# Performance work log

Measured on AMD Instinct MI355X. Metric: run time of the kernel, lower is better.

Reference implementation:

```python
import jax, jax.numpy as jnp
import numpy as np

B, T, N, K, d = 8, 12, 325, 8, 64
D = K * d


def setup_inputs() -> dict:
    key = jax.random.key(0)
    ks = jax.random.split(key, 12)
    s = 0.02
    f32 = jnp.float32
    inp = {
        "X": jax.random.normal(ks[0], (B, T, N, D), f32),
        "STE": jax.random.normal(ks[1], (B, T, N, D), f32),
        "Wq": (jax.random.normal(ks[2], (2 * D, D), f32) * s),
        "bq": jnp.zeros((D,), f32),
        "Wk": (jax.random.normal(ks[3], (2 * D, D), f32) * s),
        "bk": jnp.zeros((D,), f32),
        "Wv": (jax.random.normal(ks[4], (2 * D, D), f32) * s),
        "bv": jnp.zeros((D,), f32),
        "W1": (jax.random.normal(ks[5], (D, D), f32) * s),
        "b1": jnp.zeros((D,), f32),
        "W2": (jax.random.normal(ks[6], (D, D), f32) * s),
        "b2": jnp.zeros((D,), f32),
        "attn_mask": 0,
    }
    return inp


def reference(X, STE, Wq, bq, Wk, bk, Wv, bv, W1, b1, W2, b2, attn_mask):
    # X, STE: [B, T, N, D]
    Xc = jnp.concatenate([X, STE], axis=-1)          # [B,T,N,2D]
    q = jax.nn.relu(Xc @ Wq + bq).reshape(B, T, N, K, d)
    k = jax.nn.relu(Xc @ Wk + bk).reshape(B, T, N, K, d)
    v = jax.nn.relu(Xc @ Wv + bv).reshape(B, T, N, K, d)

    # scores: [B, K, T, N, N] (attention over spatial/node axis N)
    scores = jnp.einsum('btnhe,btmhe->bhtnm', q, k)
    # mask_flag=False -> TriangularCausalMask applied (upper-tri masked with -inf)
    causal = jnp.triu(jnp.ones((N, N), dtype=bool), 1)
    scores = jnp.where(causal, -jnp.inf, scores)
    # original scales AFTER masking; -inf / sqrt(d) stays -inf
    scores = scores / jnp.sqrt(jnp.asarray(d, scores.dtype))
    attn = jax.nn.softmax(scores, axis=-1)
    # dropout: eval mode (identity)

    ctx = jnp.einsum('bhtnm,btmhe->btnhe', attn, v).reshape(B, T, N, D)
    out = jax.nn.relu(ctx @ W1 + b1) @ W2 + b2        # [B,T,N,D]

    # match torch's head-major cat(dim=0): [K*B, T, N, N]
    attn_full = jnp.transpose(attn, (1, 0, 2, 3, 4)).reshape(K * B, T, N, N)
    return out, attn_full
```

## Files before the change

kernel.cpp:

```cpp
#include <hip/hip_runtime.h>
#include <hip/hip_bf16.h>

typedef __hip_bfloat16 bf16;
using f32x4  = __attribute__((ext_vector_type(4))) float;
using short8 = __attribute__((ext_vector_type(8))) short;

#define M_ROWS   31200
#define M_PAD    31232
#define N_TOK    325
#define D_MODEL  512
#define QKV_LD   1536
#define VTG_LD   336

#define GLOBAL_AS(p) ((const __attribute__((address_space(1))) unsigned int*)(p))
#define LDS_AS(p)    ((__attribute__((address_space(3))) unsigned int*)(p))

__global__ void init_flag(int* flag) { if (threadIdx.x == 0) *flag = 0; }

__global__ void detect_dtype(const unsigned short* __restrict__ x, int* flag)
{
    int i = blockIdx.x * 256 + threadIdx.x;
    unsigned short h = x[i];
    int e = (h >> 7) & 0xFF;
    if (e >= 135) atomicOr(flag, 1);
}

__device__ __forceinline__ float load_in(const void* p, size_t i, bool f32)
{
    return f32 ? ((const float*)p)[i] : __bfloat162float(((const bf16*)p)[i]);
}

__global__ void concat_cast(const void* __restrict__ X, const void* __restrict__ STE,
                            bf16* __restrict__ Xc, const int* __restrict__ flag)
{
    const bool f32 = (*flag != 0);
    int idx = blockIdx.x * 256 + threadIdx.x;
    int r = idx >> 7, c8 = (idx & 127) << 3;
    short8 v = {0, 0, 0, 0, 0, 0, 0, 0};
    if (r < M_ROWS) {
        const void* src = (c8 < 512) ? X : STE;
        int cc = c8 & 511;
        if (f32) {
            const float* s = (const float*)src + (size_t)r * 512 + cc;
            float4 a = *(const float4*)s;
            float4 b = *(const float4*)(s + 4);
            ((bf16*)&v)[0] = __float2bfloat16(a.x); ((bf16*)&v)[1] = __float2bfloat16(a.y);
            ((bf16*)&v)[2] = __float2bfloat16(a.z); ((bf16*)&v)[3] = __float2bfloat16(a.w);
            ((bf16*)&v)[4] = __float2bfloat16(b.x); ((bf16*)&v)[5] = __float2bfloat16(b.y);
            ((bf16*)&v)[6] = __float2bfloat16(b.z); ((bf16*)&v)[7] = __float2bfloat16(b.w);
        } else {
            v = *(const short8*)((const bf16*)src + (size_t)r * 512 + cc);
        }
    }
    *(short8*)&Xc[(size_t)r * 1024 + c8] = v;
}

__global__ void transpose_w_tiled(const void* __restrict__ src, bf16* __restrict__ dst,
                                  int krows, int ncols, const int* __restrict__ flag)
{
    __shared__ float tile[32][33];
    const bool f32 = (*flag != 0);
    const int kt = blockIdx.y * 32, nt = blockIdx.x * 32;
    const int tx = threadIdx.x & 31, ty = threadIdx.x >> 5;
#pragma unroll
    for (int r = 0; r < 32; r += 8)
        tile[ty + r][tx] = load_in(src, (size_t)(kt + ty + r) * ncols + (nt + tx), f32);
    __syncthreads();
#pragma unroll
    for (int r = 0; r < 32; r += 8)
        dst[(size_t)(nt + ty + r) * krows + (kt + tx)] = __float2bfloat16(tile[tx][ty + r]);
}

__global__ void prep_bias(const void* __restrict__ bq, const void* __restrict__ bk,
                          const void* __restrict__ bv, const void* __restrict__ b1,
                          const void* __restrict__ b2,
                          float* __restrict__ biasQKV, float* __restrict__ b1f,
                          float* __restrict__ b2f, const int* __restrict__ flag)
{
    const bool f32 = (*flag != 0);
    int i = blockIdx.x * 256 + threadIdx.x;
    if (i < 512) {
        biasQKV[i]        = load_in(bq, i, f32);
        biasQKV[512 + i]  = load_in(bk, i, f32);
        biasQKV[1024 + i] = load_in(bv, i, f32);
        b1f[i] = load_in(b1, i, f32);
        b2f[i] = load_in(b2, i, f32);
    }
}

__global__ void vt_transpose(const bf16* __restrict__ qkv, bf16* __restrict__ vtg)
{
    __shared__ bf16 vs[N_TOK * 72];
    const int t = threadIdx.x;
    const int h = blockIdx.x & 7, bt = blockIdx.x >> 3;
    const size_t rowbase = (size_t)bt * N_TOK;
    for (int task = t; task < N_TOK * 8; task += 256) {
        int m = task >> 3, e0 = (task & 7) << 3;
        *(short8*)&vs[m * 72 + e0] =
            *(const short8*)(qkv + (rowbase + m) * QKV_LD + 1024 + h * 64 + e0);
    }
    __syncthreads();
    bf16* dst = vtg + (size_t)blockIdx.x * 64 * VTG_LD;
    for (int task = t; task < 64 * VTG_LD; task += 256) {
        int e = task / VTG_LD, m = task % VTG_LD;
        dst[task] = (m < N_TOK) ? vs[m * 72 + e] : __float2bfloat16(0.f);
    }
}

template<int OUTF32, int RELU>
__global__ __launch_bounds__(512) void gemm_lds256(
    const bf16* __restrict__ A, int lda,
    const bf16* __restrict__ Bt, int ldb,
    const float* __restrict__ bias, void* __restrict__ Cv,
    int Mvalid, int Kdim, int ldc, int nby)
{
    __shared__ alignas(16) bf16 As0[256 * 32];
    __shared__ alignas(16) bf16 As1[256 * 32];
    __shared__ alignas(16) bf16 Bs0[128 * 32];
    __shared__ alignas(16) bf16 Bs1[128 * 32];
    const int cpx = gridDim.x >> 3;
    const int swz = (blockIdx.x & 7) * cpx + (blockIdx.x >> 3);
    const int m0 = (swz / nby) * 256;
    const int n0 = (swz % nby) * 128;
    const int t = threadIdx.x, wave = t >> 6, lane = t & 63;
    const int wm = (wave >> 1) * 64, wn = (wave & 1) * 64;
    const int lrow = lane & 15, lk8 = (lane >> 4) * 8;
    const int srow = lane >> 2, scol = (lane & 3) << 3;
    f32x4 acc[4][4] = {};
    const int nk = Kdim >> 6;

    for (int ks = 0; ks < nk; ++ks) {
        const int kk = ks << 6;
        __syncthreads();
#pragma unroll
        for (int c = 0; c < 2; ++c) {
            const int arow = wave * 32 + c * 16;
            const bf16* ga = A + (size_t)(m0 + arow + srow) * lda + kk + scol;
            __builtin_amdgcn_global_load_lds(GLOBAL_AS(ga),      LDS_AS(As0 + arow * 32), 16, 0, 0);
            __builtin_amdgcn_global_load_lds(GLOBAL_AS(ga + 32), LDS_AS(As1 + arow * 32), 16, 0, 0);
        }
        {
            const int brow = wave * 16;
            const bf16* gb = Bt + (size_t)(n0 + brow + srow) * ldb + kk + scol;
            __builtin_amdgcn_global_load_lds(GLOBAL_AS(gb),      LDS_AS(Bs0 + brow * 32), 16, 0, 0);
            __builtin_amdgcn_global_load_lds(GLOBAL_AS(gb + 32), LDS_AS(Bs1 + brow * 32), 16, 0, 0);
        }
        __syncthreads();
        short8 af[4], bfr[4];
#pragma unroll
        for (int i = 0; i < 4; ++i) {
            af[i]  = *(const short8*)&As0[(wm + i * 16 + lrow) * 32 + lk8];
            bfr[i] = *(const short8*)&Bs0[(wn + i * 16 + lrow) * 32 + lk8];
        }
#pragma unroll
        for (int i = 0; i < 4; ++i)
#pragma unroll
            for (int j = 0; j < 4; ++j)
                acc[i][j] = __builtin_amdgcn_mfma_f32_16x16x32_bf16(
                    af[i], bfr[j], acc[i][j], 0, 0, 0);
#pragma unroll
        for (int i = 0; i < 4; ++i) {
            af[i]  = *(const short8*)&As1[(wm + i * 16 + lrow) * 32 + lk8];
            bfr[i] = *(const short8*)&Bs1[(wn + i * 16 + lrow) * 32 + lk8];
        }
#pragma unroll
        for (int i = 0; i < 4; ++i)
#pragma unroll
            for (int j = 0; j < 4; ++j)
                acc[i][j] = __builtin_amdgcn_mfma_f32_16x16x32_bf16(
                    af[i], bfr[j], acc[i][j], 0, 0, 0);
    }

    const int r4 = (lane >> 4) * 4;
#pragma unroll
    for (int i = 0; i < 4; ++i) {
#pragma unroll
        for (int r = 0; r < 4; ++r) {
            int grow = m0 + wm + i * 16 + r4 + r;
            if (OUTF32 && grow >= Mvalid) continue;
#pragma unroll
            for (int j = 0; j < 4; ++j) {
                int gcol = n0 + wn + j * 16 + lrow;
                float v  = acc[i][j][r] + bias[gcol];
                if (RELU) v = fmaxf(v, 0.0f);
                if (OUTF32)
                    ((float*)Cv)[(size_t)grow * ldc + gcol] = v;
                else
                    ((bf16*)Cv)[(size_t)grow * ldc + gcol] = __float2bfloat16(v);
            }
        }
    }
}

#define KS_LD  72
__global__ __launch_bounds__(512) void attn_kernel(
    bf16* __restrict__ qkv, const bf16* __restrict__ vtg,
    float* __restrict__ attn_out)
{
    __shared__ alignas(16) bf16 Ks[336 * KS_LD];
    __shared__ alignas(16) bf16 ptile[8][16 * 40];
    const int t = threadIdx.x, lane = t & 63, w = t >> 6;
    const int h = blockIdx.x & 7, bt = blockIdx.x >> 3;
    const size_t rowbase = (size_t)bt * N_TOK;
    const int lrow = lane & 15, lk8 = (lane >> 4) * 8;
    const int r4 = (lane >> 4) * 4;
    const int b = bt / 12, tt2 = bt % 12;
    const size_t hb_base = (((size_t)(h * 8 + b)) * 12 + tt2) * N_TOK;
    const bf16* vt = vtg + (size_t)blockIdx.x * 64 * VTG_LD;

    for (int task = t; task < 336 * 8; task += 512) {
        int m = task >> 3, e0 = (task & 7) << 3;
        short8 v = {0, 0, 0, 0, 0, 0, 0, 0};
        if (m < N_TOK)
            v = *(const short8*)(qkv + (rowbase + m) * QKV_LD + 512 + h * 64 + e0);
        *(short8*)&Ks[m * KS_LD + e0] = v;
    }
    __syncthreads();

    for (int it = 0; it < 3; ++it) {
        if (it == 2 && w > 4) break;
        const int tile = (it < 2) ? (w + it * 8) : (20 - w);
        const int r0 = tile * 16;

        int qrow = r0 + lrow; if (qrow > N_TOK - 1) qrow = N_TOK - 1;
        const bf16* qp = qkv + (rowbase + qrow) * QKV_LD + h * 64 + lk8;
        short8 qa0 = *(const short8*)(qp);
        short8 qa1 = *(const short8*)(qp + 32);

        f32x4 f[22];
        f[21] = (f32x4){0.f, 0.f, 0.f, 0.f};
#pragma unroll
        for (int ct = 0; ct < 21; ++ct) {
            if (ct <= tile) {
                f32x4 a = {0.f, 0.f, 0.f, 0.f};
                short8 kb0 = *(const short8*)&Ks[(ct * 16 + lrow) * KS_LD + lk8];
                short8 kb1 = *(const short8*)&Ks[(ct * 16 + lrow) * KS_LD + 32 + lk8];
                a = __builtin_amdgcn_mfma_f32_16x16x32_bf16(qa0, kb0, a, 0, 0, 0);
                a = __builtin_amdgcn_mfma_f32_16x16x32_bf16(qa1, kb1, a, 0, 0, 0);
                f[ct] = a;
            }
        }

        float mx[4] = {-1e30f, -1e30f, -1e30f, -1e30f};
        float sm[4] = {0.f, 0.f, 0.f, 0.f};
#pragma unroll
        for (int ct = 0; ct < 21; ++ct) {
            if (ct <= tile) {
                const int c = ct * 16 + lrow;
#pragma unroll
                for (int r = 0; r < 4; ++r)
                    if (c <= r0 + r4 + r) mx[r] = fmaxf(mx[r], f[ct][r]);
            }
        }
#pragma unroll
        for (int r = 0; r < 4; ++r) {
#pragma unroll
            for (int o = 1; o < 16; o <<= 1) mx[r] = fmaxf(mx[r], __shfl_xor(mx[r], o));
        }
#pragma unroll
        for (int ct = 0; ct < 21; ++ct) {
            if (ct <= tile) {
                const int c = ct * 16 + lrow;
#pragma unroll
                for (int r = 0; r < 4; ++r) {
                    float e = (c <= r0 + r4 + r)
                                  ? __expf((f[ct][r] - mx[r]) * 0.125f) : 0.f;
                    f[ct][r] = e;
                    sm[r] += e;
                }
            }
        }
#pragma unroll
        for (int r = 0; r < 4; ++r) {
#pragma unroll
            for (int o = 1; o < 16; o <<= 1) sm[r] += __shfl_xor(sm[r], o);
            sm[r] = 1.0f / sm[r];
        }
#pragma unroll
        for (int ct = 0; ct < 21; ++ct) {
            if (ct <= tile) {
#pragma unroll
                for (int r = 0; r < 4; ++r) f[ct][r] *= sm[r];
            }
        }

#pragma unroll
        for (int ct = 0; ct < 21; ++ct) {
            const int c = ct * 16 + lrow;
            if (c < N_TOK) {
#pragma unroll
                for (int r = 0; r < 4; ++r) {
                    const int n = r0 + r4 + r;
                    if (n < N_TOK) {
                        float v = (ct <= tile && c <= n) ? f[ct][r] : 0.f;
                        attn_out[(hb_base + n) * N_TOK + c] = v;
                    }
                }
            }
        }

        f32x4 acc[4] = {};
        bf16* pt = &ptile[w][0];
#pragma unroll
        for (int s = 0; s < 11; ++s) {
            if (s <= (tile >> 1)) {
#pragma unroll
                for (int half = 0; half < 2; ++half) {
                    const int ct2 = 2 * s + half;
                    const int c = ct2 * 16 + lrow;
#pragma unroll
                    for (int r = 0; r < 4; ++r) {
                        const int n = r0 + r4 + r;
                        float v = (ct2 <= tile && c <= n) ? f[ct2][r] : 0.f;
                        pt[(r4 + r) * 40 + half * 16 + lrow] = __float2bfloat16(v);
                    }
                }
                short8 aa = *(const short8*)&pt[lrow * 40 + lk8];
#pragma unroll
                for (int e = 0; e < 4; ++e) {
                    short8 bb = *(const short8*)&vt[(e * 16 + lrow) * VTG_LD + s * 32 + lk8];
                    acc[e] = __builtin_amdgcn_mfma_f32_16x16x32_bf16(aa, bb, acc[e], 0, 0, 0);
                }
            }
        }

#pragma unroll
        for (int e = 0; e < 4; ++e) {
#pragma unroll
            for (int r = 0; r < 4; ++r) {
                const int n = r0 + r4 + r;
                if (n < N_TOK)
                    qkv[(rowbase + n) * QKV_LD + h * 64 + e * 16 + lrow] =
                        __float2bfloat16(acc[e][r]);
            }
        }
    }
}

extern "C" void kernel_launch(void* const* d_in, const int* in_sizes, int n_in,
                              void* d_out, int out_size, void* d_ws, size_t ws_size,
                              hipStream_t stream)
{
    const void* X   = d_in[0];
    const void* STE = d_in[1];
    const void* Wq  = d_in[2];
    const void* bq  = d_in[3];
    const void* Wk  = d_in[4];
    const void* bk  = d_in[5];
    const void* Wv  = d_in[6];
    const void* bv  = d_in[7];
    const void* W1  = d_in[8];
    const void* b1  = d_in[9];
    const void* W2  = d_in[10];
    const void* b2  = d_in[11];

    float* out0     = (float*)d_out;
    float* attn_out = (float*)d_out + (size_t)M_ROWS * D_MODEL;
    bf16*  Xc       = (bf16*)attn_out;
    bf16*  vtg      = (bf16*)d_out;

    char* ws = (char*)d_ws;
    bf16*  qkv   = (bf16*)(ws);
    bf16*  BtQKV = (bf16*)(ws + 95944704);
    bf16*  W1T   = (bf16*)(ws + 99090432);
    bf16*  W2T   = (bf16*)(ws + 99614720);
    float* biasQ = (float*)(ws + 100139008);
    float* b1f   = (float*)(ws + 100145152);
    float* b2f   = (float*)(ws + 100147200);
    int*   flag  = (int*)(ws + 100149248);
    bf16*  hbuf  = qkv + 512;

    init_flag<<<1, 64, 0, stream>>>(flag);
    detect_dtype<<<64, 256, 0, stream>>>((const unsigned short*)X, flag);

    transpose_w_tiled<<<dim3(16, 32), 256, 0, stream>>>(Wq, BtQKV, 1024, 512, flag);
    transpose_w_tiled<<<dim3(16, 32), 256, 0, stream>>>(Wk, BtQKV + 512 * 1024, 1024, 512, flag);
    transpose_w_tiled<<<dim3(16, 32), 256, 0, stream>>>(Wv, BtQKV + 1024 * 1024, 1024, 512, flag);
    transpose_w_tiled<<<dim3(16, 16), 256, 0, stream>>>(W1, W1T, 512, 512, flag);
    transpose_w_tiled<<<dim3(16, 16), 256, 0, stream>>>(W2, W2T, 512, 512, flag);
    prep_bias<<<2, 256, 0, stream>>>(bq, bk, bv, b1, b2, biasQ, b1f, b2f, flag);

    concat_cast<<<(M_PAD * 128) / 256, 256, 0, stream>>>(X, STE, Xc, flag);

    gemm_lds256<0, 1><<<122 * 12, 512, 0, stream>>>(
        Xc, 1024, BtQKV, 1024, biasQ, qkv, M_PAD, 1024, QKV_LD, 12);

    vt_transpose<<<768, 256, 0, stream>>>(qkv, vtg);

    attn_kernel<<<768, 512, 0, stream>>>(qkv, vtg, attn_out);

    gemm_lds256<0, 1><<<122 * 4, 512, 0, stream>>>(
        qkv, QKV_LD, W1T, 512, b1f, hbuf, M_PAD, 512, QKV_LD, 4);

    gemm_lds256<1, 0><<<122 * 4, 512, 0, stream>>>(
        hbuf, QKV_LD, W2T, 512, b2f, out0, M_ROWS, 512, D_MODEL, 4);
}
```

Before: 422.5 us.

## Fuse V transpose into attention kernel through shared memory

Removes the separate vt_transpose kernel, which wrote a transposed copy of V to global memory. Each attention block now loads its head's V slice straight from the qkv buffer and transposes it into a new LDS buffer, and the PV MFMA reads its B operand from there. This drops one launch and a global write-plus-read round trip. In exchange it adds about 45KB of LDS per block, which may cut blocks per CU, and the scalar transposed stores and unaligned row stride (354) risk bank conflicts and misaligned 128-bit LDS reads.

Result: faster. 374.3 us (-11.4%).

```diff
diff --git a/kernel.cpp b/kernel.cpp
--- a/kernel.cpp
+++ b/kernel.cpp
@@ -10,7 +10,6 @@
 #define N_TOK    325
 #define D_MODEL  512
 #define QKV_LD   1536
-#define VTG_LD   336
 
 #define GLOBAL_AS(p) ((const __attribute__((address_space(1))) unsigned int*)(p))
 #define LDS_AS(p)    ((__attribute__((address_space(3))) unsigned int*)(p))
@@ -88,25 +87,6 @@
     }
 }
 
-__global__ void vt_transpose(const bf16* __restrict__ qkv, bf16* __restrict__ vtg)
-{
-    __shared__ bf16 vs[N_TOK * 72];
-    const int t = threadIdx.x;
-    const int h = blockIdx.x & 7, bt = blockIdx.x >> 3;
-    const size_t rowbase = (size_t)bt * N_TOK;
-    for (int task = t; task < N_TOK * 8; task += 256) {
-        int m = task >> 3, e0 = (task & 7) << 3;
-        *(short8*)&vs[m * 72 + e0] =
-            *(const short8*)(qkv + (rowbase + m) * QKV_LD + 1024 + h * 64 + e0);
-    }
-    __syncthreads();
-    bf16* dst = vtg + (size_t)blockIdx.x * 64 * VTG_LD;
-    for (int task = t; task < 64 * VTG_LD; task += 256) {
-        int e = task / VTG_LD, m = task % VTG_LD;
-        dst[task] = (m < N_TOK) ? vs[m * 72 + e] : __float2bfloat16(0.f);
-    }
-}
-
 template<int OUTF32, int RELU>
 __global__ __launch_bounds__(512) void gemm_lds256(
     const bf16* __restrict__ A, int lda,
@@ -193,11 +173,12 @@
 }
 
 #define KS_LD  72
+#define VT_LD  354
 __global__ __launch_bounds__(512) void attn_kernel(
-    bf16* __restrict__ qkv, const bf16* __restrict__ vtg,
-    float* __restrict__ attn_out)
+    bf16* __restrict__ qkv, float* __restrict__ attn_out)
 {
     __shared__ alignas(16) bf16 Ks[336 * KS_LD];
+    __shared__ alignas(16) bf16 Vt[64 * VT_LD + 32];
     __shared__ alignas(16) bf16 ptile[8][16 * 40];
     const int t = threadIdx.x, lane = t & 63, w = t >> 6;
     const int h = blockIdx.x & 7, bt = blockIdx.x >> 3;
@@ -206,7 +187,6 @@
     const int r4 = (lane >> 4) * 4;
     const int b = bt / 12, tt2 = bt % 12;
     const size_t hb_base = (((size_t)(h * 8 + b)) * 12 + tt2) * N_TOK;
-    const bf16* vt = vtg + (size_t)blockIdx.x * 64 * VTG_LD;
 
     for (int task = t; task < 336 * 8; task += 512) {
         int m = task >> 3, e0 = (task & 7) << 3;
@@ -214,6 +194,15 @@
         if (m < N_TOK)
             v = *(const short8*)(qkv + (rowbase + m) * QKV_LD + 512 + h * 64 + e0);
         *(short8*)&Ks[m * KS_LD + e0] = v;
+    }
+    for (int task = t; task < 352 * 8; task += 512) {
+        int m = task >> 3, e0 = (task & 7) << 3;
+        short8 v = {0, 0, 0, 0, 0, 0, 0, 0};
+        if (m < N_TOK)
+            v = *(const short8*)(qkv + (rowbase + m) * QKV_LD + 1024 + h * 64 + e0);
+#pragma unroll
+        for (int j = 0; j < 8; ++j)
+            Vt[(e0 + j) * VT_LD + m] = ((bf16*)&v)[j];
     }
     __syncthreads();
 
@@ -318,7 +307,7 @@
                 short8 aa = *(const short8*)&pt[lrow * 40 + lk8];
 #pragma unroll
                 for (int e = 0; e < 4; ++e) {
-                    short8 bb = *(const short8*)&vt[(e * 16 + lrow) * VTG_LD + s * 32 + lk8];
+                    short8 bb = *(const short8*)&Vt[(e * 16 + lrow) * VT_LD + s * 32 + lk8];
                     acc[e] = __builtin_amdgcn_mfma_f32_16x16x32_bf16(aa, bb, acc[e], 0, 0, 0);
                 }
             }
@@ -357,7 +346,6 @@
     float* out0     = (float*)d_out;
     float* attn_out = (float*)d_out + (size_t)M_ROWS * D_MODEL;
     bf16*  Xc       = (bf16*)attn_out;
-    bf16*  vtg      = (bf16*)d_out;
 
     char* ws = (char*)d_ws;
     bf16*  qkv   = (bf16*)(ws);
@@ -385,9 +373,7 @@
     gemm_lds256<0, 1><<<122 * 12, 512, 0, stream>>>(
         Xc, 1024, BtQKV, 1024, biasQ, qkv, M_PAD, 1024, QKV_LD, 12);
 
-    vt_transpose<<<768, 256, 0, stream>>>(qkv, vtg);
-
-    attn_kernel<<<768, 512, 0, stream>>>(qkv, vtg, attn_out);
+    attn_kernel<<<768, 512, 0, stream>>>(qkv, attn_out);
 
     gemm_lds256<0, 1><<<122 * 4, 512, 0, stream>>>(
         qkv, QKV_LD, W1T, 512, b1f, hbuf, M_PAD, 512, QKV_LD, 4);
```
